# Kernel tuning notes

Measured on AMD Instinct MI355X. Metric: run time of the kernel, lower is better.

The kernel has to match this reference:

```python
import jax, jax.numpy as jnp
import numpy as np

EMBED = 1024
HEADS = 16
HEAD_DIM = EMBED // HEADS
EPS = 1e-5


def setup_inputs() -> dict:
    key = jax.random.key(0)
    ks = jax.random.split(key, 5)
    s = 1.0 / np.sqrt(EMBED)
    return {
        "x": jax.random.normal(ks[0], (2, 2048, EMBED), dtype=jnp.float32),
        "Wq": jax.random.normal(ks[1], (EMBED, EMBED), dtype=jnp.float32) * s,
        "Wk": jax.random.normal(ks[2], (EMBED, EMBED), dtype=jnp.float32) * s,
        "Wv": jax.random.normal(ks[3], (EMBED, EMBED), dtype=jnp.float32) * s,
        "Wout": jax.random.normal(ks[4], (EMBED, EMBED), dtype=jnp.float32) * s,
        "gamma": jnp.ones((EMBED,), dtype=jnp.float32),
        "beta": jnp.zeros((EMBED,), dtype=jnp.float32),
    }


def reference(x, Wq, Wk, Wv, Wout, gamma, beta):
    B, S, E = x.shape
    # nn.Linear(bias=False): y = x @ W.T; weight stored as [out, in]
    q = (x @ Wq.T).reshape(B, S, HEADS, HEAD_DIM)
    k = (x @ Wk.T).reshape(B, S, HEADS, HEAD_DIM)
    v = (x @ Wv.T).reshape(B, S, HEADS, HEAD_DIM)
    scale = 1.0 / jnp.sqrt(jnp.float32(HEAD_DIM)).astype(x.dtype)
    scores = jnp.einsum("bqhd,bkhd->bhqk", q, k) * scale  # [B,H,S,S]
    probs = jax.nn.softmax(scores, axis=-1)
    attn = jnp.einsum("bhqk,bkhd->bqhd", probs, v).reshape(B, S, E)
    out = attn @ Wout.T
    y = out + x
    mu = jnp.mean(y, axis=-1, keepdims=True)
    var = jnp.var(y, axis=-1, keepdims=True)
    return (y - mu) * jax.lax.rsqrt(var + EPS) * gamma + beta
```

## Files before the change

### kernel.cpp

```cpp
#include <hip/hip_runtime.h>
#include <hip/hip_bf16.h>
#include <cstdint>
#include <cstddef>

#define SEQ   2048
#define BATCH 2
#define NROWS 4096
#define EMB   1024
#define NHEAD 16
#define HD    64
#define KVBLK 64
#define NTG   16

typedef __attribute__((ext_vector_type(8))) short bf16x8;
typedef __attribute__((ext_vector_type(4))) float f32x4;
typedef __attribute__((ext_vector_type(16))) float f32x16;
typedef __attribute__((ext_vector_type(2))) int i32x2;
typedef __hip_bfloat16 bf16_t;

__device__ __forceinline__ int swz(int row, int cb) { return cb ^ ((row & 7) << 4); }

__device__ __forceinline__ void plswap(int a, int b, int& ra, int& rb) {
#if __has_builtin(__builtin_amdgcn_permlane32_swap)
  i32x2 r = __builtin_amdgcn_permlane32_swap(a, b, false, false);
  ra = r[0]; rb = r[1];
#else
  const int pa = __shfl_xor(a, 32), pb = __shfl_xor(b, 32);
  const bool lo = (threadIdx.x & 63) < 32;
  ra = lo ? a : pb;
  rb = lo ? pa : b;
#endif
}
__device__ __forceinline__ float pairmax32(float v) {
  int r0, r1;
  plswap(__float_as_int(v), __float_as_int(v), r0, r1);
  return fmaxf(__int_as_float(r0), __int_as_float(r1));
}
__device__ __forceinline__ float pairsum32(float v) {
  int r0, r1;
  plswap(__float_as_int(v), __float_as_int(v), r0, r1);
  return __int_as_float(r0) + __int_as_float(r1);
}

__global__ __launch_bounds__(256) void cast_all(const float* __restrict__ x,
                                                const float* __restrict__ a,
                                                const float* __restrict__ b,
                                                const float* __restrict__ c,
                                                const float* __restrict__ d,
                                                bf16_t* __restrict__ ox, bf16_t* __restrict__ oa,
                                                bf16_t* __restrict__ ob, bf16_t* __restrict__ oc,
                                                bf16_t* __restrict__ od) {
  const int z = blockIdx.z;
  const int n4w = EMB * EMB / 4;
  auto cvt = [](const float* in, bf16_t* out, int i) {
    float4 v = reinterpret_cast<const float4*>(in)[i];
    union { ushort4 u; bf16_t h[4]; } o;
    o.h[0] = __float2bfloat16(v.x);
    o.h[1] = __float2bfloat16(v.y);
    o.h[2] = __float2bfloat16(v.z);
    o.h[3] = __float2bfloat16(v.w);
    reinterpret_cast<ushort4*>(out)[i] = o.u;
  };
  const int base = blockIdx.x * 256 + threadIdx.x;
  if (z == 0) {
#pragma unroll
    for (int j = 0; j < 4; ++j) cvt(x, ox, j * n4w + base);
  } else {
    const float* in = (z == 1) ? a : (z == 2) ? b : (z == 3) ? c : d;
    bf16_t* out = (z == 1) ? oa : (z == 2) ? ob : (z == 3) ? oc : od;
    cvt(in, out, base);
  }
}

template <int MODE>
__device__ __forceinline__ void gemm128_body(const bf16_t* __restrict__ A,
                                             const bf16_t* __restrict__ W,
                                             bf16_t* __restrict__ Ob) {
  __shared__ __align__(16) bf16_t As[128 * 32];
  __shared__ __align__(16) bf16_t Bs[128 * 32];
  const int tid = threadIdx.x;
  const int lane = tid & 63;
  const int wv = tid >> 6;
  const int wm = wv >> 1, wn = wv & 1;
  const int brow = blockIdx.y * 128;
  const int bcol = blockIdx.x * 128;
  const int lr = lane & 15, lg = lane >> 4;

  f32x4 acc[4][4] = {};

  auto* As3 = (__attribute__((address_space(3))) char*)As;
  auto* Bs3 = (__attribute__((address_space(3))) char*)Bs;

  for (int k0 = 0; k0 < EMB; k0 += 32) {
    __syncthreads();
#pragma unroll
    for (int i = 0; i < 2; ++i) {
      const int chunk = i * 256 + tid;
      const int row = chunk >> 2;
      const int kc = (chunk & 3) * 8;
      const bf16_t* ga = A + (size_t)(brow + row) * EMB + k0 + kc;
      const bf16_t* gb = W + (size_t)(bcol + row) * EMB + k0 + kc;
      __builtin_amdgcn_global_load_lds((const __attribute__((address_space(1))) void*)ga,
                                       (__attribute__((address_space(3))) void*)(As3 + chunk * 16),
                                       16, 0, 0);
      __builtin_amdgcn_global_load_lds((const __attribute__((address_space(1))) void*)gb,
                                       (__attribute__((address_space(3))) void*)(Bs3 + chunk * 16),
                                       16, 0, 0);
    }
    __syncthreads();

    bf16x8 af[4], bfr[4];
#pragma unroll
    for (int m = 0; m < 4; ++m)
      af[m] = *reinterpret_cast<const bf16x8*>(&As[(wm * 64 + m * 16 + lr) * 32 + lg * 8]);
#pragma unroll
    for (int n = 0; n < 4; ++n)
      bfr[n] = *reinterpret_cast<const bf16x8*>(&Bs[(wn * 64 + n * 16 + lr) * 32 + lg * 8]);
#pragma unroll
    for (int m = 0; m < 4; ++m)
#pragma unroll
      for (int n = 0; n < 4; ++n)
        acc[m][n] = __builtin_amdgcn_mfma_f32_16x16x32_bf16(af[m], bfr[n], acc[m][n], 0, 0, 0);
  }

  const int r0 = brow + wm * 64;
  const int c0 = bcol + wn * 64;
#pragma unroll
  for (int m = 0; m < 4; ++m)
#pragma unroll
    for (int n = 0; n < 4; ++n) {
      if (MODE == 2) {
        const int row0 = r0 + m * 16 + lg * 4;
        const int col = c0 + n * 16 + lr;
        const size_t vt_row = (size_t)(row0 >> 11) * 1024 + col;
        const int s = row0 & 2047;
        union { uint2 u2; bf16_t h[4]; } pu;
#pragma unroll
        for (int r = 0; r < 4; ++r) pu.h[r] = __float2bfloat16(acc[m][n][r]);
        *reinterpret_cast<uint2*>(Ob + vt_row * SEQ + s) = pu.u2;
      } else {
#pragma unroll
        for (int r = 0; r < 4; ++r) {
          const int row = r0 + m * 16 + lg * 4 + r;
          const int col = c0 + n * 16 + lr;
          Ob[(size_t)row * EMB + col] = __float2bfloat16(acc[m][n][r]);
        }
      }
    }
}

__global__ __launch_bounds__(256) void gemm_qkv(const bf16_t* __restrict__ X,
                                                const bf16_t* __restrict__ Wq,
                                                const bf16_t* __restrict__ Wk,
                                                const bf16_t* __restrict__ Wv,
                                                bf16_t* __restrict__ Q,
                                                bf16_t* __restrict__ K,
                                                bf16_t* __restrict__ Vt) {
  if (blockIdx.z == 0)      gemm128_body<0>(X, Wq, Q);
  else if (blockIdx.z == 1) gemm128_body<0>(X, Wk, K);
  else                      gemm128_body<2>(X, Wv, Vt);
}

__global__ __launch_bounds__(256) void gemm_out(const bf16_t* __restrict__ Attn,
                                                const bf16_t* __restrict__ Wo,
                                                float* __restrict__ Y,
                                                const float* __restrict__ X) {
  __shared__ __align__(16) bf16_t As[128 * 32];
  __shared__ __align__(16) bf16_t Bs[64 * 32];
  const int tid = threadIdx.x;
  const int lane = tid & 63;
  const int wv = tid >> 6;
  const int wm = wv >> 1, wn = wv & 1;
  const int brow = blockIdx.y * 128;
  const int bcol = blockIdx.x * 64;
  const int lr = lane & 15, lg = lane >> 4;

  f32x4 acc[4][2] = {};

  auto* As3 = (__attribute__((address_space(3))) char*)As;
  auto* Bs3 = (__attribute__((address_space(3))) char*)Bs;

  for (int k0 = 0; k0 < EMB; k0 += 32) {
    __syncthreads();
#pragma unroll
    for (int i = 0; i < 2; ++i) {
      const int chunk = i * 256 + tid;
      const int row = chunk >> 2;
      const int kc = (chunk & 3) * 8;
      const bf16_t* ga = Attn + (size_t)(brow + row) * EMB + k0 + kc;
      __builtin_amdgcn_global_load_lds((const __attribute__((address_space(1))) void*)ga,
                                       (__attribute__((address_space(3))) void*)(As3 + chunk * 16),
                                       16, 0, 0);
    }
    {
      const int row = tid >> 2;
      const int kc = (tid & 3) * 8;
      const bf16_t* gb = Wo + (size_t)(bcol + row) * EMB + k0 + kc;
      __builtin_amdgcn_global_load_lds((const __attribute__((address_space(1))) void*)gb,
                                       (__attribute__((address_space(3))) void*)(Bs3 + tid * 16),
                                       16, 0, 0);
    }
    __syncthreads();

    bf16x8 af[4], bfr[2];
#pragma unroll
    for (int m = 0; m < 4; ++m)
      af[m] = *reinterpret_cast<const bf16x8*>(&As[(wm * 64 + m * 16 + lr) * 32 + lg * 8]);
#pragma unroll
    for (int n = 0; n < 2; ++n)
      bfr[n] = *reinterpret_cast<const bf16x8*>(&Bs[(wn * 32 + n * 16 + lr) * 32 + lg * 8]);
#pragma unroll
    for (int m = 0; m < 4; ++m)
#pragma unroll
      for (int n = 0; n < 2; ++n)
        acc[m][n] = __builtin_amdgcn_mfma_f32_16x16x32_bf16(af[m], bfr[n], acc[m][n], 0, 0, 0);
  }

  const int r0 = brow + wm * 64;
  const int c0 = bcol + wn * 32;
#pragma unroll
  for (int m = 0; m < 4; ++m)
#pragma unroll
    for (int n = 0; n < 2; ++n)
#pragma unroll
      for (int r = 0; r < 4; ++r) {
        const int row = r0 + m * 16 + lg * 4 + r;
        const int col = c0 + n * 16 + lr;
        const size_t idx = (size_t)row * EMB + col;
        Y[idx] = acc[m][n][r] + X[idx];
      }
}

__global__ __launch_bounds__(512, 4) void attn_kernel(const bf16_t* __restrict__ Q,
                                                      const bf16_t* __restrict__ K,
                                                      const bf16_t* __restrict__ Vt,
                                                      bf16_t* __restrict__ Oout) {
  __shared__ __align__(16) char L[65536];

  const int tid = threadIdx.x;
  const int lane = tid & 63;
  const int wv = tid >> 6;
  const int w = wv & 3;
  const int sg = wv >> 2;
  const int lq = lane & 31;
  const int lh = lane >> 5;

  const int f = blockIdx.x + 16 * blockIdx.y + 256 * blockIdx.z;
  const int ww = (f & 7) * 64 + (f >> 3);
  const int qb = ww & 15;
  const int h = (ww >> 4) & 15;
  const int b = ww >> 8;

  const size_t baseRow = (size_t)b * SEQ;
  const int hoff = h * HD;
  const int q0 = qb * 128 + w * 32;

  const float qscale = 0.125f * 1.44269504f;
  bf16x8 qf[4];
#pragma unroll
  for (int ks = 0; ks < 4; ++ks) {
    bf16x8 t = *reinterpret_cast<const bf16x8*>(
        &Q[(baseRow + q0 + lq) * EMB + hoff + ks * 16 + lh * 8]);
    union { bf16x8 v; bf16_t h[8]; } u;
    u.v = t;
#pragma unroll
    for (int e = 0; e < 8; ++e)
      u.h[e] = __float2bfloat16(__bfloat162float(u.h[e]) * qscale);
    qf[ks] = u.v;
  }

  f32x16 o0 = {}, o1 = {};
  float mrow = -1e30f, lrow = 0.f;

  auto* L3 = (__attribute__((address_space(3))) char*)L;
  const int gbase = sg * 32768;

  const int stid = tid & 255;
  const int srow = stid >> 3;
  const int scb = swz(srow, (stid & 7) * 16) >> 1;
  const bf16_t* kp = K + (baseRow + sg * 1024 + srow) * EMB + hoff + scb;
  const bf16_t* vp = Vt + ((size_t)(b * 1024 + hoff) + srow) * SEQ + sg * 1024 + scb;

  auto stage = [&](int buf) {
#pragma unroll
    for (int i = 0; i < 2; ++i) {
      const int c = i * 256 + stid;
      __builtin_amdgcn_global_load_lds(
          (const __attribute__((address_space(1))) void*)(kp + i * 32 * EMB),
          (__attribute__((address_space(3))) void*)(L3 + gbase + buf * 8192 + c * 16), 16, 0, 0);
      __builtin_amdgcn_global_load_lds(
          (const __attribute__((address_space(1))) void*)(vp + i * 32 * SEQ),
          (__attribute__((address_space(3))) void*)(L3 + gbase + 16384 + buf * 8192 + c * 16), 16, 0, 0);
    }
    kp += KVBLK * EMB;
    vp += KVBLK;
  };

  stage(0);
  __syncthreads();

  for (int t = 0; t < NTG; ++t) {
    const int cur = t & 1;
    if (t + 1 < NTG) stage(cur ^ 1);

    const char* Kb = (const char*)L + gbase + cur * 8192;
    const char* Vb = (const char*)L + gbase + 16384 + cur * 8192;

    f32x16 st0 = {}, st1 = {};
    __builtin_amdgcn_s_setprio(1);
#pragma unroll
    for (int ks = 0; ks < 4; ++ks) {
      bf16x8 kf0 = *reinterpret_cast<const bf16x8*>(Kb + lq * 128 + swz(lq, ks * 32 + lh * 16));
      st0 = __builtin_amdgcn_mfma_f32_32x32x16_bf16(kf0, qf[ks], st0, 0, 0, 0);
    }
#pragma unroll
    for (int ks = 0; ks < 4; ++ks) {
      bf16x8 kf1 = *reinterpret_cast<const bf16x8*>(Kb + (32 + lq) * 128 + swz(lq, ks * 32 + lh * 16));
      st1 = __builtin_amdgcn_mfma_f32_32x32x16_bf16(kf1, qf[ks], st1, 0, 0, 0);
    }
    __builtin_amdgcn_s_setprio(0);

    float mx = -1e30f;
#pragma unroll
    for (int r = 0; r < 16; ++r) mx = fmaxf(mx, st0[r]);
#pragma unroll
    for (int r = 0; r < 16; ++r) mx = fmaxf(mx, st1[r]);
    mx = pairmax32(mx);

    if (!__all(mx - mrow <= 8.f)) {
      const float mnew = fmaxf(mrow, mx);
      const float al = __builtin_amdgcn_exp2f(mrow - mnew);
      mrow = mnew;
      lrow *= al;
#pragma unroll
      for (int r = 0; r < 16; ++r) o0[r] *= al;
#pragma unroll
      for (int r = 0; r < 16; ++r) o1[r] *= al;
    }

#pragma unroll
    for (int r = 0; r < 16; ++r) st0[r] = __builtin_amdgcn_exp2f(st0[r] - mrow);
#pragma unroll
    for (int r = 0; r < 16; ++r) st1[r] = __builtin_amdgcn_exp2f(st1[r] - mrow);
    {
      float a0 = (st0[0] + st0[1]) + (st0[2] + st0[3]);
      float a1 = (st0[4] + st0[5]) + (st0[6] + st0[7]);
      float a2 = (st0[8] + st0[9]) + (st0[10] + st0[11]);
      float a3 = (st0[12] + st0[13]) + (st0[14] + st0[15]);
      float b0 = (st1[0] + st1[1]) + (st1[2] + st1[3]);
      float b1 = (st1[4] + st1[5]) + (st1[6] + st1[7]);
      float b2 = (st1[8] + st1[9]) + (st1[10] + st1[11]);
      float b3 = (st1[12] + st1[13]) + (st1[14] + st1[15]);
      lrow += pairsum32(((a0 + a1) + (a2 + a3)) + ((b0 + b1) + (b2 + b3)));
    }

    bf16x8 pb[4];
#pragma unroll
    for (int jh = 0; jh < 2; ++jh)
#pragma unroll
      for (int sub = 0; sub < 2; ++sub) {
        const f32x16& s = jh ? st1 : st0;
        int w01, w23, w45, w67;
        asm("v_cvt_pk_bf16_f32 %0, %1, %2" : "=v"(w01) : "v"(s[sub * 8 + 0]), "v"(s[sub * 8 + 1]));
        asm("v_cvt_pk_bf16_f32 %0, %1, %2" : "=v"(w23) : "v"(s[sub * 8 + 2]), "v"(s[sub * 8 + 3]));
        asm("v_cvt_pk_bf16_f32 %0, %1, %2" : "=v"(w45) : "v"(s[sub * 8 + 4]), "v"(s[sub * 8 + 5]));
        asm("v_cvt_pk_bf16_f32 %0, %1, %2" : "=v"(w67) : "v"(s[sub * 8 + 6]), "v"(s[sub * 8 + 7]));
        int d0, d1, d2, d3;
        plswap(w01, w45, d0, d2);
        plswap(w23, w67, d1, d3);
        union { int i[4]; bf16x8 v; } u;
        u.i[0] = d0; u.i[1] = d1; u.i[2] = d2; u.i[3] = d3;
        pb[jh * 2 + sub] = u.v;
      }

    __builtin_amdgcn_s_setprio(1);
#pragma unroll
    for (int js = 0; js < 4; ++js) {
      bf16x8 vf0 = *reinterpret_cast<const bf16x8*>(Vb + lq * 128 + swz(lq, js * 32 + lh * 16));
      o0 = __builtin_amdgcn_mfma_f32_32x32x16_bf16(vf0, pb[js], o0, 0, 0, 0);
    }
#pragma unroll
    for (int js = 0; js < 4; ++js) {
      bf16x8 vf1 = *reinterpret_cast<const bf16x8*>(Vb + (32 + lq) * 128 + swz(lq, js * 32 + lh * 16));
      o1 = __builtin_amdgcn_mfma_f32_32x32x16_bf16(vf1, pb[js], o1, 0, 0, 0);
    }
    __builtin_amdgcn_s_setprio(0);

    __syncthreads();
  }

  float* OL = reinterpret_cast<float*>(L + 32768);
  float2* MLx = reinterpret_cast<float2*>(L);
  __syncthreads();
  if (sg == 1) {
    MLx[w * 64 + lane] = make_float2(mrow, lrow);
#pragma unroll
    for (int r = 0; r < 16; ++r) OL[w * 2048 + r * 64 + lane] = o0[r];
#pragma unroll
    for (int r = 0; r < 16; ++r) OL[w * 2048 + (16 + r) * 64 + lane] = o1[r];
  }
  __syncthreads();
  if (sg == 0) {
    const float2 ml1 = MLx[w * 64 + lane];
    const float M = fmaxf(mrow, ml1.x);
    const float f0 = __builtin_amdgcn_exp2f(mrow - M);
    const float f1 = __builtin_amdgcn_exp2f(ml1.x - M);
    const float inv = 1.f / (f0 * lrow + f1 * ml1.y);
    const size_t orow = (baseRow + q0 + lq) * EMB + hoff;
#pragma unroll
    for (int g = 0; g < 4; ++g) {
      union { uint2 u2; bf16_t h[4]; } pu;
#pragma unroll
      for (int r = 0; r < 4; ++r)
        pu.h[r] = __float2bfloat16((f0 * o0[g * 4 + r] + f1 * OL[w * 2048 + (g * 4 + r) * 64 + lane]) * inv);
      *reinterpret_cast<uint2*>(Oout + orow + g * 8 + lh * 4) = pu.u2;
    }
#pragma unroll
    for (int g = 0; g < 4; ++g) {
      union { uint2 u2; bf16_t h[4]; } pu;
#pragma unroll
      for (int r = 0; r < 4; ++r)
        pu.h[r] = __float2bfloat16((f0 * o1[g * 4 + r] + f1 * OL[w * 2048 + (16 + g * 4 + r) * 64 + lane]) * inv);
      *reinterpret_cast<uint2*>(Oout + orow + 32 + g * 8 + lh * 4) = pu.u2;
    }
  }
}

__global__ __launch_bounds__(256) void ln_kernel(const float* __restrict__ Y,
                                                 const float* __restrict__ gamma,
                                                 const float* __restrict__ beta,
                                                 float* __restrict__ Out) {
  const int row = blockIdx.x;
  const int tid = threadIdx.x;
  const float4 v = reinterpret_cast<const float4*>(Y + (size_t)row * EMB)[tid];
  float s = v.x + v.y + v.z + v.w;
  float s2 = v.x * v.x + v.y * v.y + v.z * v.z + v.w * v.w;
#pragma unroll
  for (int m = 1; m < 64; m <<= 1) {
    s += __shfl_xor(s, m);
    s2 += __shfl_xor(s2, m);
  }
  __shared__ float ws[4], ws2[4];
  const int w = tid >> 6;
  if ((tid & 63) == 0) { ws[w] = s; ws2[w] = s2; }
  __syncthreads();
  s = ws[0] + ws[1] + ws[2] + ws[3];
  s2 = ws2[0] + ws2[1] + ws2[2] + ws2[3];
  const float mu = s * (1.f / EMB);
  const float var = s2 * (1.f / EMB) - mu * mu;
  const float rstd = rsqrtf(var + 1e-5f);
  const float4 g = reinterpret_cast<const float4*>(gamma)[tid];
  const float4 bt = reinterpret_cast<const float4*>(beta)[tid];
  float4 ov;
  ov.x = (v.x - mu) * rstd * g.x + bt.x;
  ov.y = (v.y - mu) * rstd * g.y + bt.y;
  ov.z = (v.z - mu) * rstd * g.z + bt.z;
  ov.w = (v.w - mu) * rstd * g.w + bt.w;
  reinterpret_cast<float4*>(Out + (size_t)row * EMB)[tid] = ov;
}

extern "C" void kernel_launch(void* const* d_in, const int* in_sizes, int n_in,
                              void* d_out, int out_size, void* d_ws, size_t ws_size,
                              hipStream_t stream) {
  const float* x = (const float*)d_in[0];
  const float* Wq = (const float*)d_in[1];
  const float* Wk = (const float*)d_in[2];
  const float* Wv = (const float*)d_in[3];
  const float* Wo = (const float*)d_in[4];
  const float* gamma = (const float*)d_in[5];
  const float* beta = (const float*)d_in[6];
  float* out = (float*)d_out;

  char* p = (char*)d_ws;
  const size_t sz_rows_bf = (size_t)NROWS * EMB * sizeof(bf16_t);
  const size_t sz_w_bf = (size_t)EMB * EMB * sizeof(bf16_t);
  bf16_t* xb = (bf16_t*)p; p += sz_rows_bf;
  bf16_t* wqb = (bf16_t*)p; p += sz_w_bf;
  bf16_t* wkb = (bf16_t*)p; p += sz_w_bf;
  bf16_t* wvb = (bf16_t*)p; p += sz_w_bf;
  bf16_t* wob = (bf16_t*)p; p += sz_w_bf;
  bf16_t* q = (bf16_t*)p; p += sz_rows_bf;
  bf16_t* k = (bf16_t*)p; p += sz_rows_bf;
  bf16_t* vt = (bf16_t*)p; p += sz_rows_bf;
  bf16_t* attn = (bf16_t*)p; p += sz_rows_bf;
  float* y = (float*)q;

  const int n4w = EMB * EMB / 4;
  cast_all<<<dim3(n4w / 256, 1, 5), 256, 0, stream>>>(x, Wq, Wk, Wv, Wo,
                                                      xb, wqb, wkb, wvb, wob);

  gemm_qkv<<<dim3(EMB / 128, NROWS / 128, 3), 256, 0, stream>>>(xb, wqb, wkb, wvb, q, k, vt);

  attn_kernel<<<dim3(16, 16, BATCH), 512, 0, stream>>>(q, k, vt, attn);

  gemm_out<<<dim3(EMB / 64, NROWS / 128, 1), 256, 0, stream>>>(attn, wob, y, x);

  ln_kernel<<<NROWS, 256, 0, stream>>>(y, gamma, beta, out);
}
```

Measured before the change: 119.8 us.

## Halve attention KV tile to 32 and shrink LDS for higher occupancy

The attention kernel now processes 32 keys per iteration instead of 64, halving the per-stage K/V LDS buffers to 32KB total and adding a new V swizzle for the narrower rows. The launch bound is raised from 4 to 8 blocks per CU, and the split-K merge epilogue writes o0 and o1 to LDS in two phases so it fits the smaller buffer. The aim is more resident waves and fewer registers (one score tile instead of two), at the cost of twice as many loop iterations, syncthreads and softmax rescale checks, plus extra barriers in the epilogue.

```diff
diff --git a/kernel.cpp b/kernel.cpp
--- a/kernel.cpp
+++ b/kernel.cpp
@@ -9,8 +9,8 @@
 #define EMB   1024
 #define NHEAD 16
 #define HD    64
-#define KVBLK 64
-#define NTG   16
+#define KVB   32
+#define NTG2  32
 
 typedef __attribute__((ext_vector_type(8))) short bf16x8;
 typedef __attribute__((ext_vector_type(4))) float f32x4;
@@ -19,6 +19,7 @@
 typedef __hip_bfloat16 bf16_t;
 
 __device__ __forceinline__ int swz(int row, int cb) { return cb ^ ((row & 7) << 4); }
+__device__ __forceinline__ int swzV(int row, int cb) { return cb ^ ((row & 3) << 4); }
 
 __device__ __forceinline__ void plswap(int a, int b, int& ra, int& rb) {
 #if __has_builtin(__builtin_amdgcn_permlane32_swap)
@@ -231,11 +232,11 @@
       }
 }
 
-__global__ __launch_bounds__(512, 4) void attn_kernel(const bf16_t* __restrict__ Q,
+__global__ __launch_bounds__(512, 8) void attn_kernel(const bf16_t* __restrict__ Q,
                                                       const bf16_t* __restrict__ K,
                                                       const bf16_t* __restrict__ Vt,
                                                       bf16_t* __restrict__ Oout) {
-  __shared__ __align__(16) char L[65536];
+  __shared__ __align__(16) char L[32768];
 
   const int tid = threadIdx.x;
   const int lane = tid & 63;
@@ -273,58 +274,49 @@
   float mrow = -1e30f, lrow = 0.f;
 
   auto* L3 = (__attribute__((address_space(3))) char*)L;
-  const int gbase = sg * 32768;
+  const int gbase = sg * 16384;
 
   const int stid = tid & 255;
-  const int srow = stid >> 3;
-  const int scb = swz(srow, (stid & 7) * 16) >> 1;
-  const bf16_t* kp = K + (baseRow + sg * 1024 + srow) * EMB + hoff + scb;
-  const bf16_t* vp = Vt + ((size_t)(b * 1024 + hoff) + srow) * SEQ + sg * 1024 + scb;
+  const int krow = stid >> 3;
+  const int kcb = swz(krow, (stid & 7) * 16) >> 1;
+  const bf16_t* kp = K + (baseRow + sg * 1024 + krow) * EMB + hoff + kcb;
+  const int vrow = stid >> 2;
+  const int vcb = swzV(vrow, (stid & 3) * 16) >> 1;
+  const bf16_t* vp = Vt + ((size_t)(b * 1024 + hoff) + vrow) * SEQ + sg * 1024 + vcb;
 
   auto stage = [&](int buf) {
-#pragma unroll
-    for (int i = 0; i < 2; ++i) {
-      const int c = i * 256 + stid;
-      __builtin_amdgcn_global_load_lds(
-          (const __attribute__((address_space(1))) void*)(kp + i * 32 * EMB),
-          (__attribute__((address_space(3))) void*)(L3 + gbase + buf * 8192 + c * 16), 16, 0, 0);
-      __builtin_amdgcn_global_load_lds(
-          (const __attribute__((address_space(1))) void*)(vp + i * 32 * SEQ),
-          (__attribute__((address_space(3))) void*)(L3 + gbase + 16384 + buf * 8192 + c * 16), 16, 0, 0);
-    }
-    kp += KVBLK * EMB;
-    vp += KVBLK;
+    __builtin_amdgcn_global_load_lds(
+        (const __attribute__((address_space(1))) void*)kp,
+        (__attribute__((address_space(3))) void*)(L3 + gbase + buf * 4096 + stid * 16), 16, 0, 0);
+    __builtin_amdgcn_global_load_lds(
+        (const __attribute__((address_space(1))) void*)vp,
+        (__attribute__((address_space(3))) void*)(L3 + gbase + 8192 + buf * 4096 + stid * 16), 16, 0, 0);
+    kp += KVB * EMB;
+    vp += KVB;
   };
 
   stage(0);
   __syncthreads();
 
-  for (int t = 0; t < NTG; ++t) {
+  for (int t = 0; t < NTG2; ++t) {
     const int cur = t & 1;
-    if (t + 1 < NTG) stage(cur ^ 1);
-
-    const char* Kb = (const char*)L + gbase + cur * 8192;
-    const char* Vb = (const char*)L + gbase + 16384 + cur * 8192;
-
-    f32x16 st0 = {}, st1 = {};
+    if (t + 1 < NTG2) stage(cur ^ 1);
+
+    const char* Kb = (const char*)L + gbase + cur * 4096;
+    const char* Vb = (const char*)L + gbase + 8192 + cur * 4096;
+
+    f32x16 st0 = {};
     __builtin_amdgcn_s_setprio(1);
 #pragma unroll
     for (int ks = 0; ks < 4; ++ks) {
       bf16x8 kf0 = *reinterpret_cast<const bf16x8*>(Kb + lq * 128 + swz(lq, ks * 32 + lh * 16));
       st0 = __builtin_amdgcn_mfma_f32_32x32x16_bf16(kf0, qf[ks], st0, 0, 0, 0);
     }
-#pragma unroll
-    for (int ks = 0; ks < 4; ++ks) {
-      bf16x8 kf1 = *reinterpret_cast<const bf16x8*>(Kb + (32 + lq) * 128 + swz(lq, ks * 32 + lh * 16));
-      st1 = __builtin_amdgcn_mfma_f32_32x32x16_bf16(kf1, qf[ks], st1, 0, 0, 0);
-    }
     __builtin_amdgcn_s_setprio(0);
 
     float mx = -1e30f;
 #pragma unroll
     for (int r = 0; r < 16; ++r) mx = fmaxf(mx, st0[r]);
-#pragma unroll
-    for (int r = 0; r < 16; ++r) mx = fmaxf(mx, st1[r]);
     mx = pairmax32(mx);
 
     if (!__all(mx - mrow <= 8.f)) {
@@ -340,48 +332,39 @@
 
 #pragma unroll
     for (int r = 0; r < 16; ++r) st0[r] = __builtin_amdgcn_exp2f(st0[r] - mrow);
-#pragma unroll
-    for (int r = 0; r < 16; ++r) st1[r] = __builtin_amdgcn_exp2f(st1[r] - mrow);
     {
       float a0 = (st0[0] + st0[1]) + (st0[2] + st0[3]);
       float a1 = (st0[4] + st0[5]) + (st0[6] + st0[7]);
       float a2 = (st0[8] + st0[9]) + (st0[10] + st0[11]);
       float a3 = (st0[12] + st0[13]) + (st0[14] + st0[15]);
-      float b0 = (st1[0] + st1[1]) + (st1[2] + st1[3]);
-      float b1 = (st1[4] + st1[5]) + (st1[6] + st1[7]);
-      float b2 = (st1[8] + st1[9]) + (st1[10] + st1[11]);
-      float b3 = (st1[12] + st1[13]) + (st1[14] + st1[15]);
-      lrow += pairsum32(((a0 + a1) + (a2 + a3)) + ((b0 + b1) + (b2 + b3)));
-    }
-
-    bf16x8 pb[4];
-#pragma unroll
-    for (int jh = 0; jh < 2; ++jh)
-#pragma unroll
-      for (int sub = 0; sub < 2; ++sub) {
-        const f32x16& s = jh ? st1 : st0;
-        int w01, w23, w45, w67;
-        asm("v_cvt_pk_bf16_f32 %0, %1, %2" : "=v"(w01) : "v"(s[sub * 8 + 0]), "v"(s[sub * 8 + 1]));
-        asm("v_cvt_pk_bf16_f32 %0, %1, %2" : "=v"(w23) : "v"(s[sub * 8 + 2]), "v"(s[sub * 8 + 3]));
-        asm("v_cvt_pk_bf16_f32 %0, %1, %2" : "=v"(w45) : "v"(s[sub * 8 + 4]), "v"(s[sub * 8 + 5]));
-        asm("v_cvt_pk_bf16_f32 %0, %1, %2" : "=v"(w67) : "v"(s[sub * 8 + 6]), "v"(s[sub * 8 + 7]));
-        int d0, d1, d2, d3;
-        plswap(w01, w45, d0, d2);
-        plswap(w23, w67, d1, d3);
-        union { int i[4]; bf16x8 v; } u;
-        u.i[0] = d0; u.i[1] = d1; u.i[2] = d2; u.i[3] = d3;
-        pb[jh * 2 + sub] = u.v;
-      }
+      lrow += pairsum32((a0 + a1) + (a2 + a3));
+    }
+
+    bf16x8 pb[2];
+#pragma unroll
+    for (int sub = 0; sub < 2; ++sub) {
+      int w01, w23, w45, w67;
+      asm("v_cvt_pk_bf16_f32 %0, %1, %2" : "=v"(w01) : "v"(st0[sub * 8 + 0]), "v"(st0[sub * 8 + 1]));
+      asm("v_cvt_pk_bf16_f32 %0, %1, %2" : "=v"(w23) : "v"(st0[sub * 8 + 2]), "v"(st0[sub * 8 + 3]));
+      asm("v_cvt_pk_bf16_f32 %0, %1, %2" : "=v"(w45) : "v"(st0[sub * 8 + 4]), "v"(st0[sub * 8 + 5]));
+      asm("v_cvt_pk_bf16_f32 %0, %1, %2" : "=v"(w67) : "v"(st0[sub * 8 + 6]), "v"(st0[sub * 8 + 7]));
+      int d0, d1, d2, d3;
+      plswap(w01, w45, d0, d2);
+      plswap(w23, w67, d1, d3);
+      union { int i[4]; bf16x8 v; } u;
+      u.i[0] = d0; u.i[1] = d1; u.i[2] = d2; u.i[3] = d3;
+      pb[sub] = u.v;
+    }
 
     __builtin_amdgcn_s_setprio(1);
 #pragma unroll
-    for (int js = 0; js < 4; ++js) {
-      bf16x8 vf0 = *reinterpret_cast<const bf16x8*>(Vb + lq * 128 + swz(lq, js * 32 + lh * 16));
+    for (int js = 0; js < 2; ++js) {
+      bf16x8 vf0 = *reinterpret_cast<const bf16x8*>(Vb + lq * 64 + swzV(lq, js * 32 + lh * 16));
       o0 = __builtin_amdgcn_mfma_f32_32x32x16_bf16(vf0, pb[js], o0, 0, 0, 0);
     }
 #pragma unroll
-    for (int js = 0; js < 4; ++js) {
-      bf16x8 vf1 = *reinterpret_cast<const bf16x8*>(Vb + (32 + lq) * 128 + swz(lq, js * 32 + lh * 16));
+    for (int js = 0; js < 2; ++js) {
+      bf16x8 vf1 = *reinterpret_cast<const bf16x8*>(Vb + (32 + lq) * 64 + swzV(32 + lq, js * 32 + lh * 16));
       o1 = __builtin_amdgcn_mfma_f32_32x32x16_bf16(vf1, pb[js], o1, 0, 0, 0);
     }
     __builtin_amdgcn_s_setprio(0);
@@ -389,38 +372,45 @@
     __syncthreads();
   }
 
-  float* OL = reinterpret_cast<float*>(L + 32768);
-  float2* MLx = reinterpret_cast<float2*>(L);
+  float* OL = reinterpret_cast<float*>(L);
+  float2* MLx = reinterpret_cast<float2*>(L + 16384);
+  float f0 = 1.f, f1 = 0.f, inv = 1.f;
   __syncthreads();
   if (sg == 1) {
     MLx[w * 64 + lane] = make_float2(mrow, lrow);
 #pragma unroll
-    for (int r = 0; r < 16; ++r) OL[w * 2048 + r * 64 + lane] = o0[r];
-#pragma unroll
-    for (int r = 0; r < 16; ++r) OL[w * 2048 + (16 + r) * 64 + lane] = o1[r];
-  }
-  __syncthreads();
+    for (int r = 0; r < 16; ++r) OL[w * 1024 + r * 64 + lane] = o0[r];
+  }
+  __syncthreads();
+  const size_t orow = (baseRow + q0 + lq) * EMB + hoff;
   if (sg == 0) {
     const float2 ml1 = MLx[w * 64 + lane];
     const float M = fmaxf(mrow, ml1.x);
-    const float f0 = __builtin_amdgcn_exp2f(mrow - M);
-    const float f1 = __builtin_amdgcn_exp2f(ml1.x - M);
-    const float inv = 1.f / (f0 * lrow + f1 * ml1.y);
-    const size_t orow = (baseRow + q0 + lq) * EMB + hoff;
+    f0 = __builtin_amdgcn_exp2f(mrow - M);
+    f1 = __builtin_amdgcn_exp2f(ml1.x - M);
+    inv = 1.f / (f0 * lrow + f1 * ml1.y);
 #pragma unroll
     for (int g = 0; g < 4; ++g) {
       union { uint2 u2; bf16_t h[4]; } pu;
 #pragma unroll
       for (int r = 0; r < 4; ++r)
-        pu.h[r] = __float2bfloat16((f0 * o0[g * 4 + r] + f1 * OL[w * 2048 + (g * 4 + r) * 64 + lane]) * inv);
+        pu.h[r] = __float2bfloat16((f0 * o0[g * 4 + r] + f1 * OL[w * 1024 + (g * 4 + r) * 64 + lane]) * inv);
       *reinterpret_cast<uint2*>(Oout + orow + g * 8 + lh * 4) = pu.u2;
     }
+  }
+  __syncthreads();
+  if (sg == 1) {
+#pragma unroll
+    for (int r = 0; r < 16; ++r) OL[w * 1024 + r * 64 + lane] = o1[r];
+  }
+  __syncthreads();
+  if (sg == 0) {
 #pragma unroll
     for (int g = 0; g < 4; ++g) {
       union { uint2 u2; bf16_t h[4]; } pu;
 #pragma unroll
       for (int r = 0; r < 4; ++r)
-        pu.h[r] = __float2bfloat16((f0 * o1[g * 4 + r] + f1 * OL[w * 2048 + (16 + g * 4 + r) * 64 + lane]) * inv);
+        pu.h[r] = __float2bfloat16((f0 * o1[g * 4 + r] + f1 * OL[w * 1024 + (g * 4 + r) * 64 + lane]) * inv);
       *reinterpret_cast<uint2*>(Oout + orow + 32 + g * 8 + lh * 4) = pu.u2;
     }
   }
```

After: 355.1 us. 2.97x slower.
